# Kernel optimization log

Hardware: AMD Instinct MI355X
Metric: run time of the kernel (lower is better)

The kernel has to match this reference:

```python
import jax, jax.numpy as jnp
import numpy as np

N, E, IN_DIM, HID, PROJ, NG = 50000, 1600000, 128, 128, 128, 64


def setup_inputs() -> dict:
    key = jax.random.key(0)
    ks = jax.random.split(key, 12)
    def glorot(k, fan_in, fan_out):
        s = (6.0 / (fan_in + fan_out)) ** 0.5
        return jax.random.uniform(k, (fan_in, fan_out), jnp.float32, -s, s)
    x = jax.random.normal(ks[0], (N, IN_DIM), jnp.float32)
    edge_index = jax.random.randint(ks[1], (2, E), 0, N, jnp.int32)
    batch = jnp.sort(jax.random.randint(ks[2], (N,), 0, NG, jnp.int32))
    return {
        "x": x,
        "edge_index": edge_index,
        "batch": batch,
        "num_graphs": NG,
        "W1": glorot(ks[3], IN_DIM, HID), "b1": jnp.zeros((HID,), jnp.float32),
        "W2": glorot(ks[4], HID, HID),    "b2": jnp.zeros((HID,), jnp.float32),
        "pW1": glorot(ks[5], HID, HID),   "pb1": jnp.zeros((HID,), jnp.float32),
        "pW2": glorot(ks[6], HID, PROJ),  "pb2": jnp.zeros((PROJ,), jnp.float32),
    }


def _gcn_norm(edge_index, n_nodes):
    # add self loops, compute symmetric normalization (PyG GCNConv default)
    loop = jnp.arange(n_nodes, dtype=edge_index.dtype)
    src = jnp.concatenate([edge_index[0], loop])
    dst = jnp.concatenate([edge_index[1], loop])
    deg = jax.ops.segment_sum(jnp.ones_like(dst, jnp.float32), dst, num_segments=n_nodes)
    dinv = jnp.where(deg > 0, jax.lax.rsqrt(deg), 0.0)
    norm = dinv[src] * dinv[dst]  # [E+N]
    return src, dst, norm


def _gcn_conv(h, W, b, src, dst, norm, n_nodes):
    hw = h @ W                              # [N, out]
    msg = hw[src] * norm[:, None]           # gather + scale, [E+N, out]
    out = jax.ops.segment_sum(msg, dst, num_segments=n_nodes)  # scatter-add
    return out + b


def reference(x, edge_index, batch, num_graphs, W1, b1, W2, b2, pW1, pb1, pW2, pb2):
    n_nodes = x.shape[0]
    src, dst, norm = _gcn_norm(edge_index, n_nodes)
    # conv stack (dropout is identity in eval mode)
    h = jax.nn.relu(_gcn_conv(x, W1, b1, src, dst, norm, n_nodes))
    h = jax.nn.relu(_gcn_conv(h, W2, b2, src, dst, norm, n_nodes))
    # global mean pool over graphs
    sums = jax.ops.segment_sum(h, batch, num_segments=num_graphs)
    cnts = jax.ops.segment_sum(jnp.ones((n_nodes,), h.dtype), batch, num_segments=num_graphs)
    hg = sums / jnp.maximum(cnts, 1.0)[:, None]
    # MLP projection head
    z = jax.nn.relu(hg @ pW1 + pb1) @ pW2 + pb2
    # L2 normalize (torch F.normalize with eps=1e-12)
    nrm = jnp.maximum(jnp.linalg.norm(z, axis=1, keepdims=True), 1e-12)
    return z / nrm
```

## Files before the change

### kernel.cpp

```cpp
#include <hip/hip_runtime.h>
#include <cstdint>
#include <cstddef>


using short8 = __attribute__((ext_vector_type(8))) short;
using f32x4v = __attribute__((ext_vector_type(4))) float;


static __device__ __forceinline__ unsigned f2bf_rne(float f) {
    unsigned u = __float_as_uint(f);
    return (u + 0x7FFFu + ((u >> 16) & 1u)) >> 16;
}
static __device__ __forceinline__ unsigned pack_bf2(float lo, float hi) {
    return f2bf_rne(lo) | (f2bf_rne(hi) << 16);
}
static __device__ __forceinline__ float bf_lo(unsigned v) {
    return __uint_as_float(v << 16);
}
static __device__ __forceinline__ float bf_hi(unsigned v) {
    return __uint_as_float(v & 0xFFFF0000u);
}


__global__ void k_bincount(const int* __restrict__ dst, int* __restrict__ bcnt,
                           int E, int NB) {
    __shared__ int h[256];
    int t = threadIdx.x;
    h[t] = 0;
    __syncthreads();
    int base_i = blockIdx.x * 4096;
#pragma unroll
    for (int j = 0; j < 16; ++j) {
        int i = base_i + j * 256 + t;
        if (i < E) atomicAdd(&h[dst[i] >> 8], 1);
    }
    __syncthreads();
    if (t < NB && h[t]) atomicAdd(&bcnt[t], h[t]);
}

__global__ void k_bscan(const int* __restrict__ bcnt, int* __restrict__ bbase,
                        int* __restrict__ bcur, int NB) {
    __shared__ int s[256];
    int t = threadIdx.x;
    int v = (t < NB) ? bcnt[t] : 0;
    s[t] = v;
    __syncthreads();
    for (int d = 1; d < 256; d <<= 1) {
        int x = (t >= d) ? s[t - d] : 0;
        __syncthreads();
        s[t] += x;
        __syncthreads();
    }
    if (t < NB) {
        int excl = s[t] - v;
        bbase[t] = excl;
        bcur[t]  = excl;
        if (t == NB - 1) bbase[NB] = s[t];
    }
}


__global__ void k_bin(const int* __restrict__ src, const int* __restrict__ dst,
                      int* __restrict__ bcur, int* __restrict__ bkt,
                      int E, int NB) {
    __shared__ int cnt[256];
    __shared__ int pos[256];
    int t = threadIdx.x;
    int base_i = blockIdx.x * 4096;

    cnt[t] = 0;
    __syncthreads();

    int b_[16];
    int v_[16];
#pragma unroll
    for (int j = 0; j < 16; ++j) {
        int i = base_i + j * 256 + t;
        if (i < E) {
            int s = src[i], d = dst[i];
            v_[j] = s | ((d & 255) << 16);
            int b = d >> 8;
            b_[j] = b;
            atomicAdd(&cnt[b], 1);
        } else {
            b_[j] = -1;
        }
    }
    __syncthreads();

    if (t < NB) {
        int c = cnt[t];
        pos[t] = c ? atomicAdd(&bcur[t], c) : 0;
    }
    __syncthreads();

#pragma unroll
    for (int j = 0; j < 16; ++j) {
        if (b_[j] >= 0) {
            int p = atomicAdd(&pos[b_[j]], 1);
            bkt[p] = v_[j];
        }
    }
}


__global__ void k_fill2(const int* __restrict__ bkt, const int* __restrict__ bbase,
                        int* __restrict__ off, float* __restrict__ dinv,
                        int* __restrict__ csr, int N, int E, int NB) {
    __shared__ int hist[256];
    __shared__ int loff[256];
    __shared__ int cur[256];
    int b = blockIdx.x, t = threadIdx.x;
    if (t < 256) hist[t] = 0;
    __syncthreads();

    int e0 = bbase[b], e1 = bbase[b + 1];
    for (int i = e0 + t; i < e1; i += 1024)
        atomicAdd(&hist[(bkt[i] >> 16) & 255], 1);
    __syncthreads();

    if (t < 256) loff[t] = hist[t];
    __syncthreads();
    for (int d = 1; d < 256; d <<= 1) {
        int x = 0;
        if (t < 256 && t >= d) x = loff[t - d];
        __syncthreads();
        if (t < 256) loff[t] += x;
        __syncthreads();
    }

    if (t < 256) {
        int n = (b << 8) + t;
        if (n < N) {
            int base = e0 + loff[t] - hist[t];
            off[n]  = base;
            cur[t]  = base;
            dinv[n] = rsqrtf((float)(hist[t] + 1));
        }
    }
    if (b == NB - 1 && t == 0) off[N] = E;
    __syncthreads();

    for (int i = e0 + t; i < e1; i += 1024) {
        int v  = bkt[i];
        int dl = (v >> 16) & 255;
        int p  = atomicAdd(&cur[dl], 1);
        csr[p] = v & 0xFFFF;
    }
}


template<bool BF16IN>
__global__ __launch_bounds__(256) void k_gemm(
        const void* __restrict__ in_, const float* __restrict__ W,
        const float* __restrict__ dinv, unsigned* __restrict__ outbf, int N) {
    __shared__ __align__(16) char smem[34816];
    unsigned short* wbf = (unsigned short*)smem;
    float*          sCf = (float*)smem;

    int t = threadIdx.x;
    int w  = t >> 6;
    int l  = t & 63;
    int lo = l & 15;
    int hi = l >> 4;

#pragma unroll
    for (int i = 0; i < 16; ++i) {
        int idx = (i * 256 + t) * 4;
        float4 wv = *reinterpret_cast<const float4*>(W + idx);
        int k = idx >> 7, c = idx & 127;
        wbf[(c    ) * 136 + k] = (unsigned short)f2bf_rne(wv.x);
        wbf[(c + 1) * 136 + k] = (unsigned short)f2bf_rne(wv.y);
        wbf[(c + 2) * 136 + k] = (unsigned short)f2bf_rne(wv.z);
        wbf[(c + 3) * 136 + k] = (unsigned short)f2bf_rne(wv.w);
    }
    __syncthreads();

    int rbase = blockIdx.x * 64 + w * 16;
    int row   = rbase + lo;
    int rowc  = (row < N) ? row : (N - 1);

    short8 a[4];
    if constexpr (BF16IN) {
        const uint4* pu = (const uint4*)in_;
#pragma unroll
        for (int ks = 0; ks < 4; ++ks)
            a[ks] = __builtin_bit_cast(short8, pu[(size_t)rowc * 16 + ks * 4 + hi]);
    } else {
        const float4* pf = (const float4*)in_;
#pragma unroll
        for (int ks = 0; ks < 4; ++ks) {
            float4 fA = pf[(size_t)rowc * 32 + ks * 8 + hi * 2];
            float4 fB = pf[(size_t)rowc * 32 + ks * 8 + hi * 2 + 1];
            short8 s;
            s[0] = (short)f2bf_rne(fA.x); s[1] = (short)f2bf_rne(fA.y);
            s[2] = (short)f2bf_rne(fA.z); s[3] = (short)f2bf_rne(fA.w);
            s[4] = (short)f2bf_rne(fB.x); s[5] = (short)f2bf_rne(fB.y);
            s[6] = (short)f2bf_rne(fB.z); s[7] = (short)f2bf_rne(fB.w);
            a[ks] = s;
        }
    }

    f32x4v acc[8];
#pragma unroll
    for (int i = 0; i < 8; ++i) acc[i] = (f32x4v){0.f, 0.f, 0.f, 0.f};

#pragma unroll
    for (int cp = 0; cp < 2; ++cp) {
        short8 b[4][4];
#pragma unroll
        for (int ct = 0; ct < 4; ++ct) {
            int col = cp * 64 + ct * 16 + lo;
#pragma unroll
            for (int ks = 0; ks < 4; ++ks)
                b[ct][ks] = *reinterpret_cast<const short8*>(
                    &wbf[col * 136 + ks * 32 + hi * 8]);
        }
#pragma unroll
        for (int ks = 0; ks < 4; ++ks)
#pragma unroll
            for (int ct = 0; ct < 4; ++ct)
                acc[cp * 4 + ct] = __builtin_amdgcn_mfma_f32_16x16x32_bf16(
                    a[ks], b[ct][ks], acc[cp * 4 + ct], 0, 0, 0);
    }
    __syncthreads();

#pragma unroll
    for (int i = 0; i < 8; ++i) {
        int colb = (i >> 2) * 64 + (i & 3) * 16 + lo;
#pragma unroll
        for (int r = 0; r < 4; ++r)
            sCf[(w * 16 + hi * 4 + r) * 132 + colb] = acc[i][r];
    }
    __syncthreads();

    if (row < N) {
        float d = dinv[rowc];
#pragma unroll
        for (int j = 0; j < 4; ++j) {
            float4 fA = *reinterpret_cast<const float4*>(
                &sCf[(w * 16 + lo) * 132 + hi * 32 + j * 8]);
            float4 fB = *reinterpret_cast<const float4*>(
                &sCf[(w * 16 + lo) * 132 + hi * 32 + j * 8 + 4]);
            uint4 o = { pack_bf2(fA.x * d, fA.y * d), pack_bf2(fA.z * d, fA.w * d),
                        pack_bf2(fB.x * d, fB.y * d), pack_bf2(fB.z * d, fB.w * d) };
            reinterpret_cast<uint4*>(outbf)[(size_t)row * 16 + hi * 4 + j] = o;
        }
    }
}


__global__ void k_aggr(const unsigned* __restrict__ hw, const int* __restrict__ off,
                       const int* __restrict__ csr, const float* __restrict__ dinv,
                       const float* __restrict__ bias, unsigned* __restrict__ out, int N) {
    int wid  = (blockIdx.x * blockDim.x + threadIdx.x) >> 6;
    int lane = threadIdx.x & 63;
    if (wid >= N) return;
    int n  = wid;
    int q  = lane >> 4;
    int li = lane & 15;

    const uint4* hw4 = reinterpret_cast<const uint4*>(hw);

    float a0 = 0.f, a1 = 0.f, a2 = 0.f, a3 = 0.f;
    float a4 = 0.f, a5 = 0.f, a6 = 0.f, a7 = 0.f;
    if (q == 0) {
        uint4 v = hw4[(unsigned)(n << 4) + li];
        a0 = bf_lo(v.x); a1 = bf_hi(v.x);
        a2 = bf_lo(v.y); a3 = bf_hi(v.y);
        a4 = bf_lo(v.z); a5 = bf_hi(v.z);
        a6 = bf_lo(v.w); a7 = bf_hi(v.w);
    }

#define ACC8(v) \
    a0 += bf_lo(v.x); a1 += bf_hi(v.x); \
    a2 += bf_lo(v.y); a3 += bf_hi(v.y); \
    a4 += bf_lo(v.z); a5 += bf_hi(v.z); \
    a6 += bf_lo(v.w); a7 += bf_hi(v.w);

    int e = off[n], e1 = off[n + 1];
    while (e < e1) {
        int rem = e1 - e;
        int cnt = rem < 64 ? rem : 64;
        int s_l = N;
        if (lane < cnt) s_l = csr[e + lane];
        int jn = (cnt + 3) >> 2;
        int j = 0;
        for (; j + 8 <= jn; j += 8) {
            int s0 = __shfl(s_l, 4 * j + q);
            int s1 = __shfl(s_l, 4 * j + 4 + q);
            int s2 = __shfl(s_l, 4 * j + 8 + q);
            int s3 = __shfl(s_l, 4 * j + 12 + q);
            int s4 = __shfl(s_l, 4 * j + 16 + q);
            int s5 = __shfl(s_l, 4 * j + 20 + q);
            int s6 = __shfl(s_l, 4 * j + 24 + q);
            int s7 = __shfl(s_l, 4 * j + 28 + q);
            uint4 v0 = hw4[(unsigned)(s0 << 4) + li];
            uint4 v1 = hw4[(unsigned)(s1 << 4) + li];
            uint4 v2 = hw4[(unsigned)(s2 << 4) + li];
            uint4 v3 = hw4[(unsigned)(s3 << 4) + li];
            uint4 v4 = hw4[(unsigned)(s4 << 4) + li];
            uint4 v5 = hw4[(unsigned)(s5 << 4) + li];
            uint4 v6 = hw4[(unsigned)(s6 << 4) + li];
            uint4 v7 = hw4[(unsigned)(s7 << 4) + li];
            ACC8(v0) ACC8(v1) ACC8(v2) ACC8(v3)
            ACC8(v4) ACC8(v5) ACC8(v6) ACC8(v7)
        }
        for (; j + 4 <= jn; j += 4) {
            int s0 = __shfl(s_l, 4 * j + q);
            int s1 = __shfl(s_l, 4 * j + 4 + q);
            int s2 = __shfl(s_l, 4 * j + 8 + q);
            int s3 = __shfl(s_l, 4 * j + 12 + q);
            uint4 v0 = hw4[(unsigned)(s0 << 4) + li];
            uint4 v1 = hw4[(unsigned)(s1 << 4) + li];
            uint4 v2 = hw4[(unsigned)(s2 << 4) + li];
            uint4 v3 = hw4[(unsigned)(s3 << 4) + li];
            ACC8(v0) ACC8(v1) ACC8(v2) ACC8(v3)
        }
        for (; j < jn; ++j) {
            int   s = __shfl(s_l, 4 * j + q);
            uint4 v = hw4[(unsigned)(s << 4) + li];
            ACC8(v)
        }
        e += cnt;
    }
#undef ACC8

    int p1 = (lane + 32) & 63;
    a0 += __shfl(a0, p1); a1 += __shfl(a1, p1);
    a2 += __shfl(a2, p1); a3 += __shfl(a3, p1);
    a4 += __shfl(a4, p1); a5 += __shfl(a5, p1);
    a6 += __shfl(a6, p1); a7 += __shfl(a7, p1);
    int p2 = (lane + 16) & 63;
    a0 += __shfl(a0, p2); a1 += __shfl(a1, p2);
    a2 += __shfl(a2, p2); a3 += __shfl(a3, p2);
    a4 += __shfl(a4, p2); a5 += __shfl(a5, p2);
    a6 += __shfl(a6, p2); a7 += __shfl(a7, p2);

    if (q == 0) {
        float di = dinv[n];
        const float4* b4 = reinterpret_cast<const float4*>(bias);
        float4 bA = b4[2 * li], bB = b4[2 * li + 1];
        a0 = fmaxf(fmaf(a0, di, bA.x), 0.f); a1 = fmaxf(fmaf(a1, di, bA.y), 0.f);
        a2 = fmaxf(fmaf(a2, di, bA.z), 0.f); a3 = fmaxf(fmaf(a3, di, bA.w), 0.f);
        a4 = fmaxf(fmaf(a4, di, bB.x), 0.f); a5 = fmaxf(fmaf(a5, di, bB.y), 0.f);
        a6 = fmaxf(fmaf(a6, di, bB.z), 0.f); a7 = fmaxf(fmaf(a7, di, bB.w), 0.f);
        uint4 r = { pack_bf2(a0, a1), pack_bf2(a2, a3),
                    pack_bf2(a4, a5), pack_bf2(a6, a7) };
        reinterpret_cast<uint4*>(out)[(unsigned)(n << 4) + li] = r;
    }
}


__global__ void k_pool(const unsigned* __restrict__ h, const int* __restrict__ batch,
                       float* __restrict__ pooled, int* __restrict__ cnt,
                       int N, int npw) {
    int wid  = (blockIdx.x * blockDim.x + threadIdx.x) >> 6;
    int lane = threadIdx.x & 63;
    int n0 = wid * npw;
    if (n0 >= N) return;
    int n1 = n0 + npw; if (n1 > N) n1 = N;

    float ax = 0.f, ay = 0.f;
    int g = batch[n0];
    int c = 0;
    for (int n = n0; n < n1; ++n) {
        int gn = batch[n];
        if (gn != g) {
            atomicAdd(&pooled[g * 128 + 2 * lane],     ax);
            atomicAdd(&pooled[g * 128 + 2 * lane + 1], ay);
            if (lane == 0) atomicAdd(&cnt[g], c);
            ax = 0.f; ay = 0.f; c = 0; g = gn;
        }
        unsigned v = h[(size_t)n * 64 + lane];
        ax += bf_lo(v); ay += bf_hi(v); ++c;
    }
    atomicAdd(&pooled[g * 128 + 2 * lane],     ax);
    atomicAdd(&pooled[g * 128 + 2 * lane + 1], ay);
    if (lane == 0) atomicAdd(&cnt[g], c);
}


__global__ void k_head(const float* __restrict__ pooled, const int* __restrict__ cnt,
                       const float* __restrict__ pW1, const float* __restrict__ pb1,
                       const float* __restrict__ pW2, const float* __restrict__ pb2,
                       float* __restrict__ out) {
    __shared__ float hg[128];
    __shared__ float z1[128];
    __shared__ float red[128];
    int g = blockIdx.x, t = threadIdx.x;

    float c = fmaxf((float)cnt[g], 1.0f);
    hg[t] = pooled[g * 128 + t] / c;
    __syncthreads();

    float a = pb1[t];
#pragma unroll 8
    for (int k = 0; k < 128; ++k) a = fmaf(hg[k], pW1[k * 128 + t], a);
    z1[t] = fmaxf(a, 0.f);
    __syncthreads();

    float z = pb2[t];
#pragma unroll 8
    for (int k = 0; k < 128; ++k) z = fmaf(z1[k], pW2[k * 128 + t], z);

    red[t] = z * z;
    __syncthreads();
    for (int d = 64; d > 0; d >>= 1) {
        if (t < d) red[t] += red[t + d];
        __syncthreads();
    }
    float nrm = fmaxf(sqrtf(red[0]), 1e-12f);
    out[g * 128 + t] = z / nrm;
}


extern "C" void kernel_launch(void* const* d_in, const int* in_sizes, int n_in,
                              void* d_out, int out_size, void* d_ws, size_t ws_size,
                              hipStream_t stream) {
    const float* x    = (const float*)d_in[0];
    const int*   eidx = (const int*)  d_in[1];
    const int*   batch= (const int*)  d_in[2];
    const float* W1   = (const float*)d_in[4];
    const float* b1   = (const float*)d_in[5];
    const float* W2   = (const float*)d_in[6];
    const float* b2   = (const float*)d_in[7];
    const float* pW1  = (const float*)d_in[8];
    const float* pb1  = (const float*)d_in[9];
    const float* pW2  = (const float*)d_in[10];
    const float* pb2  = (const float*)d_in[11];
    float* out = (float*)d_out;

    const int N  = in_sizes[0] / 128;
    const int E  = in_sizes[1] / 2;
    const int NG = out_size / 128;
    const int NB = (N + 255) >> 8;

    const int* src = eidx;
    const int* dst = eidx + E;

    char* p = (char*)d_ws;
    auto alloc = [&](size_t bytes) -> void* {
        void* r = (void*)p;
        p += (bytes + 255) & ~(size_t)255;
        return r;
    };
    int*      bcnt     = (int*)     alloc((size_t)NB * 4);
    int*      bbase    = (int*)     alloc((size_t)(NB + 1) * 4);
    int*      bcur     = (int*)     alloc((size_t)NB * 4);
    int*      off      = (int*)     alloc((size_t)(N + 1) * 4);
    float*    dinv     = (float*)   alloc((size_t)N * 4);
    int*      bkt      = (int*)     alloc((size_t)E * 4);
    int*      csr      = (int*)     alloc((size_t)E * 4);
    unsigned* bufH     = (unsigned*)alloc((size_t)(N + 1) * 64 * 4);
    unsigned* bufB     = (unsigned*)alloc((size_t)N * 64 * 4);
    float*    pooled   = (float*)   alloc((size_t)NG * 128 * 4);
    int*      cnt      = (int*)     alloc((size_t)NG * 4);

    const int tB = (E + 4095) / 4096;

    hipMemsetAsync(bcnt,   0, (size_t)NB * 4, stream);
    hipMemsetAsync(bufH + (size_t)N * 64, 0, 256, stream);
    hipMemsetAsync(pooled, 0, (size_t)NG * 128 * 4, stream);
    hipMemsetAsync(cnt,    0, (size_t)NG * 4, stream);

    k_bincount<<<tB, 256, 0, stream>>>(dst, bcnt, E, NB);
    k_bscan   <<<1, 256, 0, stream>>>(bcnt, bbase, bcur, NB);
    k_bin     <<<tB, 256, 0, stream>>>(src, dst, bcur, bkt, E, NB);
    k_fill2   <<<NB, 1024, 0, stream>>>(bkt, bbase, off, dinv, csr, N, E, NB);

    const int gB = (N + 63) / 64;
    const int aB = (N + 3) / 4;

    k_gemm<false><<<gB, 256, 0, stream>>>((const void*)x, W1, dinv, bufH, N);
    k_aggr<<<aB, 256, 0, stream>>>(bufH, off, csr, dinv, b1, bufB, N);
    k_gemm<true><<<gB, 256, 0, stream>>>((const void*)bufB, W2, dinv, bufH, N);
    k_aggr<<<aB, 256, 0, stream>>>(bufH, off, csr, dinv, b2, bufB, N);

    const int NPW = 32;
    const int waves = (N + NPW - 1) / NPW;
    const int pB = (waves * 64 + 255) / 256;
    k_pool<<<pB, 256, 0, stream>>>(bufB, batch, pooled, cnt, N, NPW);

    k_head<<<NG, 128, 0, stream>>>(pooled, cnt, pW1, pb1, pW2, pb2, out);
}
```

Measured before the change: 237.9 us.

## Process two row tiles per GEMM block and store results directly without LDS staging

Each GEMM block now handles two 64-row tiles, which halves how often the weight matrix is converted into LDS. The epilogue drops the LDS transpose and its barriers, writing each bf16 element straight to global memory as a 2-byte scattered store. The zero-initialised workspace buffers are placed next to each other so one memset replaces three. The direct 16-bit stores are poorly coalesced compared with the earlier 16-byte row stores, which may cost more write bandwidth than the LDS round trip saved.

```diff
diff --git a/kernel.cpp b/kernel.cpp
--- a/kernel.cpp
+++ b/kernel.cpp
@@ -154,9 +154,7 @@
 __global__ __launch_bounds__(256) void k_gemm(
         const void* __restrict__ in_, const float* __restrict__ W,
         const float* __restrict__ dinv, unsigned* __restrict__ outbf, int N) {
-    __shared__ __align__(16) char smem[34816];
-    unsigned short* wbf = (unsigned short*)smem;
-    float*          sCf = (float*)smem;
+    __shared__ unsigned short wbf[128 * 136];
 
     int t = threadIdx.x;
     int w  = t >> 6;
@@ -176,75 +174,71 @@
     }
     __syncthreads();
 
-    int rbase = blockIdx.x * 64 + w * 16;
-    int row   = rbase + lo;
-    int rowc  = (row < N) ? row : (N - 1);
-
-    short8 a[4];
-    if constexpr (BF16IN) {
-        const uint4* pu = (const uint4*)in_;
-#pragma unroll
-        for (int ks = 0; ks < 4; ++ks)
-            a[ks] = __builtin_bit_cast(short8, pu[(size_t)rowc * 16 + ks * 4 + hi]);
-    } else {
-        const float4* pf = (const float4*)in_;
-#pragma unroll
-        for (int ks = 0; ks < 4; ++ks) {
-            float4 fA = pf[(size_t)rowc * 32 + ks * 8 + hi * 2];
-            float4 fB = pf[(size_t)rowc * 32 + ks * 8 + hi * 2 + 1];
-            short8 s;
-            s[0] = (short)f2bf_rne(fA.x); s[1] = (short)f2bf_rne(fA.y);
-            s[2] = (short)f2bf_rne(fA.z); s[3] = (short)f2bf_rne(fA.w);
-            s[4] = (short)f2bf_rne(fB.x); s[5] = (short)f2bf_rne(fB.y);
-            s[6] = (short)f2bf_rne(fB.z); s[7] = (short)f2bf_rne(fB.w);
-            a[ks] = s;
-        }
-    }
-
-    f32x4v acc[8];
-#pragma unroll
-    for (int i = 0; i < 8; ++i) acc[i] = (f32x4v){0.f, 0.f, 0.f, 0.f};
-
-#pragma unroll
-    for (int cp = 0; cp < 2; ++cp) {
-        short8 b[4][4];
-#pragma unroll
-        for (int ct = 0; ct < 4; ++ct) {
-            int col = cp * 64 + ct * 16 + lo;
+    unsigned short* outS = (unsigned short*)outbf;
+
+#pragma unroll
+    for (int tt = 0; tt < 2; ++tt) {
+        int rbase = (blockIdx.x * 2 + tt) * 64 + w * 16;
+        if (rbase >= N) continue;
+        int row  = rbase + lo;
+        int rowc = (row < N) ? row : (N - 1);
+
+        short8 a[4];
+        if constexpr (BF16IN) {
+            const uint4* pu = (const uint4*)in_;
 #pragma unroll
             for (int ks = 0; ks < 4; ++ks)
-                b[ct][ks] = *reinterpret_cast<const short8*>(
-                    &wbf[col * 136 + ks * 32 + hi * 8]);
-        }
-#pragma unroll
-        for (int ks = 0; ks < 4; ++ks)
-#pragma unroll
-            for (int ct = 0; ct < 4; ++ct)
-                acc[cp * 4 + ct] = __builtin_amdgcn_mfma_f32_16x16x32_bf16(
-                    a[ks], b[ct][ks], acc[cp * 4 + ct], 0, 0, 0);
-    }
-    __syncthreads();
-
-#pragma unroll
-    for (int i = 0; i < 8; ++i) {
-        int colb = (i >> 2) * 64 + (i & 3) * 16 + lo;
-#pragma unroll
-        for (int r = 0; r < 4; ++r)
-            sCf[(w * 16 + hi * 4 + r) * 132 + colb] = acc[i][r];
-    }
-    __syncthreads();
-
-    if (row < N) {
-        float d = dinv[rowc];
-#pragma unroll
-        for (int j = 0; j < 4; ++j) {
-            float4 fA = *reinterpret_cast<const float4*>(
-                &sCf[(w * 16 + lo) * 132 + hi * 32 + j * 8]);
-            float4 fB = *reinterpret_cast<const float4*>(
-                &sCf[(w * 16 + lo) * 132 + hi * 32 + j * 8 + 4]);
-            uint4 o = { pack_bf2(fA.x * d, fA.y * d), pack_bf2(fA.z * d, fA.w * d),
-                        pack_bf2(fB.x * d, fB.y * d), pack_bf2(fB.z * d, fB.w * d) };
-            reinterpret_cast<uint4*>(outbf)[(size_t)row * 16 + hi * 4 + j] = o;
+                a[ks] = __builtin_bit_cast(short8, pu[(size_t)rowc * 16 + ks * 4 + hi]);
+        } else {
+            const float4* pf = (const float4*)in_;
+#pragma unroll
+            for (int ks = 0; ks < 4; ++ks) {
+                float4 fA = pf[(size_t)rowc * 32 + ks * 8 + hi * 2];
+                float4 fB = pf[(size_t)rowc * 32 + ks * 8 + hi * 2 + 1];
+                short8 s;
+                s[0] = (short)f2bf_rne(fA.x); s[1] = (short)f2bf_rne(fA.y);
+                s[2] = (short)f2bf_rne(fA.z); s[3] = (short)f2bf_rne(fA.w);
+                s[4] = (short)f2bf_rne(fB.x); s[5] = (short)f2bf_rne(fB.y);
+                s[6] = (short)f2bf_rne(fB.z); s[7] = (short)f2bf_rne(fB.w);
+                a[ks] = s;
+            }
+        }
+
+        f32x4v acc[8];
+#pragma unroll
+        for (int i = 0; i < 8; ++i) acc[i] = (f32x4v){0.f, 0.f, 0.f, 0.f};
+
+#pragma unroll
+        for (int cp = 0; cp < 2; ++cp) {
+            short8 b[4][4];
+#pragma unroll
+            for (int ct = 0; ct < 4; ++ct) {
+                int col = cp * 64 + ct * 16 + lo;
+#pragma unroll
+                for (int ks = 0; ks < 4; ++ks)
+                    b[ct][ks] = *reinterpret_cast<const short8*>(
+                        &wbf[col * 136 + ks * 32 + hi * 8]);
+            }
+#pragma unroll
+            for (int ks = 0; ks < 4; ++ks)
+#pragma unroll
+                for (int ct = 0; ct < 4; ++ct)
+                    acc[cp * 4 + ct] = __builtin_amdgcn_mfma_f32_16x16x32_bf16(
+                        a[ks], b[ct][ks], acc[cp * 4 + ct], 0, 0, 0);
+        }
+
+#pragma unroll
+        for (int r = 0; r < 4; ++r) {
+            int orow = rbase + hi * 4 + r;
+            if (orow < N) {
+                float d = dinv[orow];
+#pragma unroll
+                for (int i = 0; i < 8; ++i) {
+                    int colb = (i >> 2) * 64 + (i & 3) * 16 + lo;
+                    outS[(size_t)orow * 128 + colb] =
+                        (unsigned short)f2bf_rne(acc[i][r] * d);
+                }
+            }
         }
     }
 }
@@ -445,7 +439,11 @@
         p += (bytes + 255) & ~(size_t)255;
         return r;
     };
+    char* zstart = p;
     int*      bcnt     = (int*)     alloc((size_t)NB * 4);
+    int*      cnt      = (int*)     alloc((size_t)NG * 4);
+    float*    pooled   = (float*)   alloc((size_t)NG * 128 * 4);
+    size_t zbytes = (size_t)(p - zstart);
     int*      bbase    = (int*)     alloc((size_t)(NB + 1) * 4);
     int*      bcur     = (int*)     alloc((size_t)NB * 4);
     int*      off      = (int*)     alloc((size_t)(N + 1) * 4);
@@ -454,23 +452,21 @@
     int*      csr      = (int*)     alloc((size_t)E * 4);
     unsigned* bufH     = (unsigned*)alloc((size_t)(N + 1) * 64 * 4);
     unsigned* bufB     = (unsigned*)alloc((size_t)N * 64 * 4);
-    float*    pooled   = (float*)   alloc((size_t)NG * 128 * 4);
-    int*      cnt      = (int*)     alloc((size_t)NG * 4);
+    (void)ws_size;
 
     const int tB = (E + 4095) / 4096;
 
-    hipMemsetAsync(bcnt,   0, (size_t)NB * 4, stream);
+    hipMemsetAsync(zstart, 0, zbytes, stream);
     hipMemsetAsync(bufH + (size_t)N * 64, 0, 256, stream);
-    hipMemsetAsync(pooled, 0, (size_t)NG * 128 * 4, stream);
-    hipMemsetAsync(cnt,    0, (size_t)NG * 4, stream);
 
     k_bincount<<<tB, 256, 0, stream>>>(dst, bcnt, E, NB);
     k_bscan   <<<1, 256, 0, stream>>>(bcnt, bbase, bcur, NB);
     k_bin     <<<tB, 256, 0, stream>>>(src, dst, bcur, bkt, E, NB);
     k_fill2   <<<NB, 1024, 0, stream>>>(bkt, bbase, off, dinv, csr, N, E, NB);
 
-    const int gB = (N + 63) / 64;
-    const int aB = (N + 3) / 4;
+    const int nrt = (N + 63) / 64;
+    const int gB  = (nrt + 1) / 2;
+    const int aB  = (N + 3) / 4;
 
     k_gemm<false><<<gB, 256, 0, stream>>>((const void*)x, W1, dinv, bufH, N);
     k_aggr<<<aB, 256, 0, stream>>>(bufH, off, csr, dinv, b1, bufB, N);
```

New measurement: 221.9 us. 6.7% less time.
